# Optimization experiments

Hardware: AMD Instinct MI355X
Metric: run time of the kernel (lower is better)

## Reference

```python
import jax, jax.numpy as jnp
import numpy as np

EPS = 1e-5
TOPK_FRAC = 0.3
MIP = 16


def conv1x1(y, w, b):
    # y: (B, Cin, L, 1); w: (Cout, Cin); b: (Cout,)
    return jnp.einsum('oc,bclw->bolw', w, y) + b[None, :, None, None]


def mdca(x, conv1_w, conv1_b, bn_gamma, bn_beta, bn_mean, bn_var,
         convh_w, convh_b, convw_w, convw_b, convd1_w, convd1_b, convd2_w, convd2_b):
    B, C, H, W = x.shape
    x_h = jnp.mean(x, axis=3, keepdims=True)                       # (B,C,H,1)
    x_w = jnp.mean(x, axis=2, keepdims=True).transpose(0, 1, 3, 2)  # (B,C,W,1)
    x_d1 = jnp.rot90(x, k=-1, axes=(2, 3))                          # (B,C,W,H)
    x_d1 = jnp.mean(x_d1, axis=2, keepdims=True)                    # (B,C,1,H)
    x_d1 = jnp.rot90(x_d1, k=1, axes=(2, 3))                        # (B,C,H,1)
    x_d2 = jnp.rot90(x, k=1, axes=(2, 3))                           # (B,C,W,H)
    x_d2 = jnp.mean(x_d2, axis=2, keepdims=True)                    # (B,C,1,H)
    x_d2 = jnp.rot90(x_d2, k=-1, axes=(2, 3))                       # (B,C,H,1) -> size W along dim2 since H==W
    y = jnp.concatenate([x_h, x_w, x_d1, x_d2], axis=2)             # (B,C,H+W+H+W,1)
    y = conv1x1(y, conv1_w, conv1_b)                                # (B,mip,2H+2W,1)
    # BatchNorm (inference form with running stats)
    inv = jax.lax.rsqrt(bn_var + EPS)
    y = (y - bn_mean[None, :, None, None]) * (bn_gamma * inv)[None, :, None, None] + bn_beta[None, :, None, None]
    y = jax.nn.relu(y)
    xh, xw, xd1, xd2 = jnp.split(y, np.cumsum([H, W, H])[:3].tolist(), axis=2)
    xw = xw.transpose(0, 1, 3, 2)    # (B,mip,1,W)
    xd1 = xd1.transpose(0, 1, 3, 2)  # (B,mip,1,H)
    xd2 = xd2.transpose(0, 1, 3, 2)  # (B,mip,1,W)
    a_h = jax.nn.sigmoid(conv1x1(xh, convh_w, convh_b))    # (B,1,H,1)
    a_w = jax.nn.sigmoid(conv1x1(xw, convw_w, convw_b))    # (B,1,1,W)
    a_d1 = jax.nn.sigmoid(conv1x1(xd1, convd1_w, convd1_b))  # (B,1,1,H)
    a_d2 = jax.nn.sigmoid(conv1x1(xd2, convd2_w, convd2_b))  # (B,1,1,W)
    # broadcasting reproduces expand(-1,-1,H,-1); valid since H == W
    importance = a_w * a_h * a_d1 * a_d2                    # (B,1,H,W)
    return importance


def reference(x, conv1_w, conv1_b, bn_gamma, bn_beta, bn_mean, bn_var,
              convh_w, convh_b, convw_w, convw_b, convd1_w, convd1_b,
              convd2_w, convd2_b, sparsity_mask):
    B, C, H, W = x.shape
    imp = mdca(x, conv1_w, conv1_b, bn_gamma, bn_beta, bn_mean, bn_var,
               convh_w, convh_b, convw_w, convw_b, convd1_w, convd1_b, convd2_w, convd2_b)
    imp_flat = imp.reshape(B, -1)                               # (B,N)
    N = imp_flat.shape[1]
    scores = imp_flat[:, :, None] * imp_flat[:, None, :]        # (B,N,N) outer product
    scores = scores * jax.nn.sigmoid(sparsity_mask)
    k = max(1, int(N * TOPK_FRAC))
    vals, idx = jax.lax.top_k(scores, k)                        # (B,N,k)
    sparse = jnp.zeros_like(scores).at[
        jnp.arange(B)[:, None, None], jnp.arange(N)[None, :, None], idx
    ].set(vals)
    attn = jax.nn.softmax(sparse, axis=-1)                      # (B,N,N)
    x_seq = x.reshape(B, C, N).transpose(0, 2, 1)               # (B,N,C)
    out_seq = attn @ x_seq                                      # (B,N,C)
    return out_seq.transpose(0, 2, 1).reshape(B, C, H, W)


def setup_inputs():
    key = jax.random.key(0)
    ks = jax.random.split(key, 8)
    B, C, H, W = 2, 256, 64, 64
    s = 0.05
    return {
        'x': jax.random.normal(ks[0], (B, C, H, W), jnp.float32),
        'conv1_w': jax.random.normal(ks[1], (MIP, C), jnp.float32) * s,
        'conv1_b': jnp.zeros((MIP,), jnp.float32),
        'bn_gamma': jnp.ones((MIP,), jnp.float32),
        'bn_beta': jnp.zeros((MIP,), jnp.float32),
        'bn_mean': jnp.zeros((MIP,), jnp.float32),
        'bn_var': jnp.ones((MIP,), jnp.float32),
        'convh_w': jax.random.normal(ks[2], (1, MIP), jnp.float32) * s,
        'convh_b': jnp.zeros((1,), jnp.float32),
        'convw_w': jax.random.normal(ks[3], (1, MIP), jnp.float32) * s,
        'convw_b': jnp.zeros((1,), jnp.float32),
        'convd1_w': jax.random.normal(ks[4], (1, MIP), jnp.float32) * s,
        'convd1_b': jnp.zeros((1,), jnp.float32),
        'convd2_w': jax.random.normal(ks[5], (1, MIP), jnp.float32) * s,
        'convd2_b': jnp.zeros((1,), jnp.float32),
        'sparsity_mask': jnp.zeros((), jnp.float32),
    }
```

## Files before the change

### kernel.cpp

```cpp
#include <hip/hip_runtime.h>

#define B_ 2
#define C_ 256
#define HW_ 64
#define N_ 4096
#define K_SEL 1228
#define MIP_ 16

__device__ __forceinline__ float sigm(float z) { return 1.0f / (1.0f + expf(-z)); }

__global__ __launch_bounds__(256) void k_pre(const float* __restrict__ x,
                                             float* __restrict__ xhT) {
  __shared__ float rp[64][17];
  __shared__ float cp[16][65];
  int bc = blockIdx.x, t = threadIdx.x;
  int b = bc >> 8, c = bc & 255;
  const float* src = x + (size_t)bc * N_;
  int g = t >> 4, b16 = t & 15;
  float c0 = 0, c1 = 0, c2 = 0, c3 = 0;
  #pragma unroll
  for (int it = 0; it < 4; ++it) {
    int row = it * 16 + g;
    float4 v = *(const float4*)&src[row * 64 + b16 * 4];
    rp[row][b16] = v.x + v.y + v.z + v.w;
    c0 += v.x; c1 += v.y; c2 += v.z; c3 += v.w;
  }
  cp[g][b16 * 4 + 0] = c0;
  cp[g][b16 * 4 + 1] = c1;
  cp[g][b16 * 4 + 2] = c2;
  cp[g][b16 * 4 + 3] = c3;
  __syncthreads();
  if (t < 64) {
    float rs = 0;
    #pragma unroll
    for (int i = 0; i < 16; ++i) rs += rp[t][i];
    xhT[(((b * 2 + 0) * 64 + t) << 8) + c] = rs * (1.0f / 64.0f);
    float cs = 0;
    #pragma unroll
    for (int gg = 0; gg < 16; ++gg) cs += cp[gg][t];
    xhT[(((b * 2 + 1) * 64 + t) << 8) + c] = cs * (1.0f / 64.0f);
  }
}

__global__ __launch_bounds__(64) void k_conv(
    const float* __restrict__ xhT,
    const float* __restrict__ w1, const float* __restrict__ b1,
    const float* __restrict__ gam, const float* __restrict__ bet,
    const float* __restrict__ mea, const float* __restrict__ var,
    const float* __restrict__ wh, const float* __restrict__ bh,
    const float* __restrict__ ww, const float* __restrict__ bw,
    const float* __restrict__ wd1, const float* __restrict__ bd1,
    const float* __restrict__ wd2, const float* __restrict__ bd2,
    float* __restrict__ ahb, float* __restrict__ swb, float* __restrict__ sdb) {
  int blk = blockIdx.x;
  int l = threadIdx.x;
  const float* yrow = xhT + ((size_t)blk << 8);
  float4 v = *(const float4*)&yrow[l * 4];
  float r[MIP_];
  #pragma unroll
  for (int o = 0; o < MIP_; ++o) {
    float4 wv = *(const float4*)&w1[o * C_ + l * 4];
    float p = fmaf(v.x, wv.x, fmaf(v.y, wv.y, fmaf(v.z, wv.z, v.w * wv.w)));
    #pragma unroll
    for (int off = 32; off; off >>= 1) p += __shfl_xor(p, off, 64);
    r[o] = p;
  }
  float aH = bh[0], aW = bw[0], aD1 = bd1[0], aD2 = bd2[0];
  #pragma unroll
  for (int o = 0; o < MIP_; ++o) {
    float sc = gam[o] * rsqrtf(var[o] + 1e-5f);
    float y = r[o] + b1[o] - mea[o];
    float rr = fmaxf(fmaf(y, sc, bet[o]), 0.0f);
    aH = fmaf(wh[o], rr, aH);
    aW = fmaf(ww[o], rr, aW);
    aD1 = fmaf(wd1[o], rr, aD1);
    aD2 = fmaf(wd2[o], rr, aD2);
  }
  if (l == 0) {
    int seg = (blk >> 6) & 1, b = blk >> 7, pos = blk & 63;
    if (seg == 0) {
      ahb[b * HW_ + pos] = sigm(aH);
      sdb[b * HW_ + pos] = sigm(aD1) * sigm(aD2);
    } else {
      swb[b * HW_ + pos] = sigm(aW);
    }
  }
}

__global__ __launch_bounds__(256) void k_sel(
    const float* __restrict__ ahb, const float* __restrict__ swb,
    const float* __restrict__ sdb, const float* __restrict__ msk,
    float* __restrict__ fs, float2* __restrict__ ad) {
  __shared__ float ahs[HW_], sps[HW_];
  __shared__ int icomb[4];
  __shared__ float fmn[4], fmx[4];
  __shared__ float qpart[7][4];
  __shared__ float qsh[7];
  int b = blockIdx.x, t = threadIdx.x;
  if (t < HW_) {
    ahs[t] = ahb[b * HW_ + t];
    sps[t] = swb[b * HW_ + t] * sdb[b * HW_ + t];
  }
  __syncthreads();

  float v[16];
  #pragma unroll
  for (int k = 0; k < 16; ++k) {
    int j = k * 256 + t;
    v[k] = ahs[j >> 6] * sps[j & 63];
  }

  float mn = v[0], mx = v[0];
  #pragma unroll
  for (int k = 1; k < 16; ++k) { mn = fminf(mn, v[k]); mx = fmaxf(mx, v[k]); }
  #pragma unroll
  for (int o = 32; o; o >>= 1) {
    mn = fminf(mn, __shfl_xor(mn, o, 64));
    mx = fmaxf(mx, __shfl_xor(mx, o, 64));
  }
  if ((t & 63) == 0) { fmn[t >> 6] = mn; fmx[t >> 6] = mx; }
  __syncthreads();
  mn = fminf(fminf(fmn[0], fmn[1]), fminf(fmn[2], fmn[3]));
  mx = fmaxf(fmaxf(fmx[0], fmx[1]), fmaxf(fmx[2], fmx[3]));
  __syncthreads();

  unsigned lo = __float_as_uint(mn);
  unsigned hi = __float_as_uint(mx) + 1u;
  while (hi - lo > 8192u) {
    unsigned mid = lo + ((hi - lo) >> 1);
    float midf = __uint_as_float(mid);
    int cnt = 0;
    #pragma unroll
    for (int k = 0; k < 16; ++k) cnt += (v[k] >= midf) ? 1 : 0;
    #pragma unroll
    for (int o = 32; o; o >>= 1) cnt += __shfl_xor(cnt, o, 64);
    if ((t & 63) == 0) icomb[t >> 6] = cnt;
    __syncthreads();
    int total = icomb[0] + icomb[1] + icomb[2] + icomb[3];
    __syncthreads();
    if (total >= K_SEL) lo = mid; else hi = mid;
  }
  float thr = __uint_as_float(lo);
  float gm = sigm(msk[0]);

  float qm[7] = {0, 0, 0, 0, 0, 0, 0};
  float* fsb = fs + b * N_;
  #pragma unroll
  for (int k = 0; k < 16; ++k) {
    int j = k * 256 + t;
    float vv = v[k];
    bool sel = vv >= thr;
    fsb[j] = sel ? vv : 0.0f;
    if (sel) {
      float p = vv;
      qm[0] += p; p *= vv;
      qm[1] += p; p *= vv;
      qm[2] += p; p *= vv;
      qm[3] += p; p *= vv;
      qm[4] += p; p *= vv;
      qm[5] += p; p *= vv;
      qm[6] += p;
    }
  }
  #pragma unroll
  for (int m = 0; m < 7; ++m) {
    float s = qm[m];
    #pragma unroll
    for (int o = 32; o; o >>= 1) s += __shfl_xor(s, o, 64);
    if ((t & 63) == 0) qpart[m][t >> 6] = s;
  }
  __syncthreads();
  if (t < 7) {
    const float invf[7] = {1.0f, 0.5f, 1.0f / 6.0f, 1.0f / 24.0f,
                           1.0f / 120.0f, 1.0f / 720.0f, 1.0f / 5040.0f};
    qsh[t] = (qpart[t][0] + qpart[t][1] + qpart[t][2] + qpart[t][3]) * invf[t];
  }
  __syncthreads();

  float q1 = qsh[0], q2 = qsh[1], q3 = qsh[2], q4 = qsh[3];
  float q5 = qsh[4], q6 = qsh[5], q7 = qsh[6];
  float2* adb = ad + b * N_;
  #pragma unroll
  for (int k = 0; k < 16; ++k) {
    int j = k * 256 + t;
    float alpha = gm * v[k];
    float h = q7;
    h = fmaf(alpha, h, q6);
    h = fmaf(alpha, h, q5);
    h = fmaf(alpha, h, q4);
    h = fmaf(alpha, h, q3);
    h = fmaf(alpha, h, q2);
    h = fmaf(alpha, h, q1);
    float denom = fmaf(alpha, h, (float)N_);
    adb[j] = make_float2(alpha, 1.0f / denom);
  }
}

__global__ __launch_bounds__(256) void k_fin(const float* __restrict__ x,
                                             const float* __restrict__ fs,
                                             const float2* __restrict__ ad,
                                             float* __restrict__ out) {
  __shared__ float part[8][4];
  __shared__ float ps[8];
  int bc = blockIdx.x, b = bc >> 8, t = threadIdx.x;
  const float* xr = x + (size_t)bc * N_;
  const float* fr = fs + (size_t)b * N_;
  float pm[8] = {0, 0, 0, 0, 0, 0, 0, 0};
  #pragma unroll
  for (int it = 0; it < 4; ++it) {
    int j = it * 1024 + t * 4;
    float4 xv = *(const float4*)&xr[j];
    float4 fv = *(const float4*)&fr[j];
    const float xe[4] = {xv.x, xv.y, xv.z, xv.w};
    const float fe[4] = {fv.x, fv.y, fv.z, fv.w};
    #pragma unroll
    for (int e = 0; e < 4; ++e) {
      float xx = xe[e], vv = fe[e];
      pm[0] += xx;
      float p = vv;
      pm[1] = fmaf(p, xx, pm[1]); p *= vv;
      pm[2] = fmaf(p, xx, pm[2]); p *= vv;
      pm[3] = fmaf(p, xx, pm[3]); p *= vv;
      pm[4] = fmaf(p, xx, pm[4]); p *= vv;
      pm[5] = fmaf(p, xx, pm[5]); p *= vv;
      pm[6] = fmaf(p, xx, pm[6]); p *= vv;
      pm[7] = fmaf(p, xx, pm[7]);
    }
  }
  #pragma unroll
  for (int m = 0; m < 8; ++m) {
    float s = pm[m];
    #pragma unroll
    for (int o = 32; o; o >>= 1) s += __shfl_xor(s, o, 64);
    if ((t & 63) == 0) part[m][t >> 6] = s;
  }
  __syncthreads();
  if (t < 8) {
    const float invf[8] = {1.0f, 1.0f, 0.5f, 1.0f / 6.0f, 1.0f / 24.0f,
                           1.0f / 120.0f, 1.0f / 720.0f, 1.0f / 5040.0f};
    ps[t] = (part[t][0] + part[t][1] + part[t][2] + part[t][3]) * invf[t];
  }
  __syncthreads();
  float T = ps[0];
  float p1 = ps[1], p2 = ps[2], p3 = ps[3], p4 = ps[4];
  float p5 = ps[5], p6 = ps[6], p7 = ps[7];
  const float2* adb = ad + (size_t)b * N_;
  float* ob = out + (size_t)bc * N_;
  #pragma unroll 4
  for (int it = 0; it < 16; ++it) {
    int i = it * 256 + t;
    float2 a = adb[i];
    float h = p7;
    h = fmaf(a.x, h, p6);
    h = fmaf(a.x, h, p5);
    h = fmaf(a.x, h, p4);
    h = fmaf(a.x, h, p3);
    h = fmaf(a.x, h, p2);
    h = fmaf(a.x, h, p1);
    ob[i] = fmaf(a.x, h, T) * a.y;
  }
}

extern "C" void kernel_launch(void* const* d_in, const int* in_sizes, int n_in,
                              void* d_out, int out_size, void* d_ws, size_t ws_size,
                              hipStream_t stream) {
  (void)in_sizes; (void)n_in; (void)out_size; (void)ws_size;
  const float* x   = (const float*)d_in[0];
  const float* w1  = (const float*)d_in[1];
  const float* b1  = (const float*)d_in[2];
  const float* gam = (const float*)d_in[3];
  const float* bet = (const float*)d_in[4];
  const float* mea = (const float*)d_in[5];
  const float* var = (const float*)d_in[6];
  const float* wh  = (const float*)d_in[7];
  const float* bh  = (const float*)d_in[8];
  const float* ww  = (const float*)d_in[9];
  const float* bw  = (const float*)d_in[10];
  const float* wd1 = (const float*)d_in[11];
  const float* bd1 = (const float*)d_in[12];
  const float* wd2 = (const float*)d_in[13];
  const float* bd2 = (const float*)d_in[14];
  const float* msk = (const float*)d_in[15];
  float* out = (float*)d_out;

  float* ws  = (float*)d_ws;
  float* xhT = ws;
  float* ahb = ws + 65536;
  float* swb = ahb + 128;
  float* sdb = swb + 128;
  float* fs  = sdb + 128;
  float2* ad = (float2*)(fs + 8192);

  hipLaunchKernelGGL(k_pre, dim3(B_ * C_), dim3(256), 0, stream, x, xhT);
  hipLaunchKernelGGL(k_conv, dim3(B_ * 2 * HW_), dim3(64), 0, stream,
                     xhT, w1, b1, gam, bet, mea, var,
                     wh, bh, ww, bw, wd1, bd1, wd2, bd2, ahb, swb, sdb);
  hipLaunchKernelGGL(k_sel, dim3(B_), dim3(256), 0, stream,
                     ahb, swb, sdb, msk, fs, ad);
  hipLaunchKernelGGL(k_fin, dim3(B_ * C_), dim3(256), 0, stream,
                     x, fs, ad, out);
}
```

Before: 28.86 us.

## Fuse top-k selection kernel into final output kernel, recomputing threshold per block

Removes the separate two-block selection kernel and its fs/ad workspace round trips. Each of the 512 output blocks now rebuilds the 4096 importance values from the small per-row vectors, runs the binary-search threshold itself, and accumulates both the denominator and numerator moment sums in one pass over x. The output is written as float4 with a direct division. This trades one launch and a serial 2-block stage for redundant binary-search work and extra barriers in every block.

```diff
diff --git a/kernel.cpp b/kernel.cpp
--- a/kernel.cpp
+++ b/kernel.cpp
@@ -87,28 +87,41 @@
   }
 }
 
-__global__ __launch_bounds__(256) void k_sel(
+__global__ __launch_bounds__(256) void k_fin(
+    const float* __restrict__ x,
     const float* __restrict__ ahb, const float* __restrict__ swb,
     const float* __restrict__ sdb, const float* __restrict__ msk,
-    float* __restrict__ fs, float2* __restrict__ ad) {
+    float* __restrict__ out) {
   __shared__ float ahs[HW_], sps[HW_];
   __shared__ int icomb[4];
   __shared__ float fmn[4], fmx[4];
-  __shared__ float qpart[7][4];
-  __shared__ float qsh[7];
-  int b = blockIdx.x, t = threadIdx.x;
+  __shared__ float red[15][4];
+  __shared__ float ps[15];
+  int bc = blockIdx.x, b = bc >> 8, t = threadIdx.x;
+  const float* xr = x + (size_t)bc * N_;
+
+  float4 xv[4];
+  #pragma unroll
+  for (int it = 0; it < 4; ++it)
+    xv[it] = *(const float4*)&xr[it * 1024 + t * 4];
+
   if (t < HW_) {
     ahs[t] = ahb[b * HW_ + t];
     sps[t] = swb[b * HW_ + t] * sdb[b * HW_ + t];
   }
   __syncthreads();
 
+  float4 sp4 = *(const float4*)&sps[(t * 4) & 63];
+  const float spe[4] = {sp4.x, sp4.y, sp4.z, sp4.w};
+  float ahv[4];
+  #pragma unroll
+  for (int it = 0; it < 4; ++it) ahv[it] = ahs[it * 16 + (t >> 4)];
+
   float v[16];
   #pragma unroll
-  for (int k = 0; k < 16; ++k) {
-    int j = k * 256 + t;
-    v[k] = ahs[j >> 6] * sps[j & 63];
-  }
+  for (int it = 0; it < 4; ++it)
+    #pragma unroll
+    for (int e = 0; e < 4; ++e) v[it * 4 + e] = ahv[it] * spe[e];
 
   float mn = v[0], mx = v[0];
   #pragma unroll
@@ -122,7 +135,6 @@
   __syncthreads();
   mn = fminf(fminf(fmn[0], fmn[1]), fminf(fmn[2], fmn[3]));
   mx = fmaxf(fmaxf(fmx[0], fmx[1]), fmaxf(fmx[2], fmx[3]));
-  __syncthreads();
 
   unsigned lo = __float_as_uint(mn);
   unsigned hi = __float_as_uint(mx) + 1u;
@@ -143,121 +155,85 @@
   float thr = __uint_as_float(lo);
   float gm = sigm(msk[0]);
 
-  float qm[7] = {0, 0, 0, 0, 0, 0, 0};
-  float* fsb = fs + b * N_;
-  #pragma unroll
-  for (int k = 0; k < 16; ++k) {
-    int j = k * 256 + t;
-    float vv = v[k];
-    bool sel = vv >= thr;
-    fsb[j] = sel ? vv : 0.0f;
-    if (sel) {
-      float p = vv;
-      qm[0] += p; p *= vv;
-      qm[1] += p; p *= vv;
-      qm[2] += p; p *= vv;
-      qm[3] += p; p *= vv;
-      qm[4] += p; p *= vv;
-      qm[5] += p; p *= vv;
-      qm[6] += p;
+  float acc[15];
+  #pragma unroll
+  for (int m = 0; m < 15; ++m) acc[m] = 0.0f;
+  #pragma unroll
+  for (int it = 0; it < 4; ++it) {
+    const float xe[4] = {xv[it].x, xv[it].y, xv[it].z, xv[it].w};
+    #pragma unroll
+    for (int e = 0; e < 4; ++e) {
+      float vv = v[it * 4 + e];
+      float xx = xe[e];
+      acc[7] += xx;
+      if (vv >= thr) {
+        float p = vv;
+        acc[0] += p;
+        acc[8] = fmaf(p, xx, acc[8]); p *= vv;
+        acc[1] += p;
+        acc[9] = fmaf(p, xx, acc[9]); p *= vv;
+        acc[2] += p;
+        acc[10] = fmaf(p, xx, acc[10]); p *= vv;
+        acc[3] += p;
+        acc[11] = fmaf(p, xx, acc[11]); p *= vv;
+        acc[4] += p;
+        acc[12] = fmaf(p, xx, acc[12]); p *= vv;
+        acc[5] += p;
+        acc[13] = fmaf(p, xx, acc[13]); p *= vv;
+        acc[6] += p;
+        acc[14] = fmaf(p, xx, acc[14]);
+      }
     }
   }
   #pragma unroll
-  for (int m = 0; m < 7; ++m) {
-    float s = qm[m];
+  for (int m = 0; m < 15; ++m) {
+    float s = acc[m];
     #pragma unroll
     for (int o = 32; o; o >>= 1) s += __shfl_xor(s, o, 64);
-    if ((t & 63) == 0) qpart[m][t >> 6] = s;
-  }
-  __syncthreads();
-  if (t < 7) {
-    const float invf[7] = {1.0f, 0.5f, 1.0f / 6.0f, 1.0f / 24.0f,
-                           1.0f / 120.0f, 1.0f / 720.0f, 1.0f / 5040.0f};
-    qsh[t] = (qpart[t][0] + qpart[t][1] + qpart[t][2] + qpart[t][3]) * invf[t];
-  }
-  __syncthreads();
-
-  float q1 = qsh[0], q2 = qsh[1], q3 = qsh[2], q4 = qsh[3];
-  float q5 = qsh[4], q6 = qsh[5], q7 = qsh[6];
-  float2* adb = ad + b * N_;
-  #pragma unroll
-  for (int k = 0; k < 16; ++k) {
-    int j = k * 256 + t;
-    float alpha = gm * v[k];
-    float h = q7;
-    h = fmaf(alpha, h, q6);
-    h = fmaf(alpha, h, q5);
-    h = fmaf(alpha, h, q4);
-    h = fmaf(alpha, h, q3);
-    h = fmaf(alpha, h, q2);
-    h = fmaf(alpha, h, q1);
-    float denom = fmaf(alpha, h, (float)N_);
-    adb[j] = make_float2(alpha, 1.0f / denom);
-  }
-}
-
-__global__ __launch_bounds__(256) void k_fin(const float* __restrict__ x,
-                                             const float* __restrict__ fs,
-                                             const float2* __restrict__ ad,
-                                             float* __restrict__ out) {
-  __shared__ float part[8][4];
-  __shared__ float ps[8];
-  int bc = blockIdx.x, b = bc >> 8, t = threadIdx.x;
-  const float* xr = x + (size_t)bc * N_;
-  const float* fr = fs + (size_t)b * N_;
-  float pm[8] = {0, 0, 0, 0, 0, 0, 0, 0};
+    if ((t & 63) == 0) red[m][t >> 6] = s;
+  }
+  __syncthreads();
+  if (t < 15) {
+    const float invf[15] = {1.0f, 0.5f, 1.0f / 6.0f, 1.0f / 24.0f,
+                            1.0f / 120.0f, 1.0f / 720.0f, 1.0f / 5040.0f,
+                            1.0f,
+                            1.0f, 0.5f, 1.0f / 6.0f, 1.0f / 24.0f,
+                            1.0f / 120.0f, 1.0f / 720.0f, 1.0f / 5040.0f};
+    ps[t] = (red[t][0] + red[t][1] + red[t][2] + red[t][3]) * invf[t];
+  }
+  __syncthreads();
+  float q1 = ps[0], q2 = ps[1], q3 = ps[2], q4 = ps[3];
+  float q5 = ps[4], q6 = ps[5], q7 = ps[6];
+  float T = ps[7];
+  float p1 = ps[8], p2 = ps[9], p3 = ps[10], p4 = ps[11];
+  float p5 = ps[12], p6 = ps[13], p7 = ps[14];
+
+  float* ob = out + (size_t)bc * N_;
   #pragma unroll
   for (int it = 0; it < 4; ++it) {
-    int j = it * 1024 + t * 4;
-    float4 xv = *(const float4*)&xr[j];
-    float4 fv = *(const float4*)&fr[j];
-    const float xe[4] = {xv.x, xv.y, xv.z, xv.w};
-    const float fe[4] = {fv.x, fv.y, fv.z, fv.w};
+    float o4[4];
     #pragma unroll
     for (int e = 0; e < 4; ++e) {
-      float xx = xe[e], vv = fe[e];
-      pm[0] += xx;
-      float p = vv;
-      pm[1] = fmaf(p, xx, pm[1]); p *= vv;
-      pm[2] = fmaf(p, xx, pm[2]); p *= vv;
-      pm[3] = fmaf(p, xx, pm[3]); p *= vv;
-      pm[4] = fmaf(p, xx, pm[4]); p *= vv;
-      pm[5] = fmaf(p, xx, pm[5]); p *= vv;
-      pm[6] = fmaf(p, xx, pm[6]); p *= vv;
-      pm[7] = fmaf(p, xx, pm[7]);
+      float alpha = gm * v[it * 4 + e];
+      float hn = p7;
+      hn = fmaf(alpha, hn, p6);
+      hn = fmaf(alpha, hn, p5);
+      hn = fmaf(alpha, hn, p4);
+      hn = fmaf(alpha, hn, p3);
+      hn = fmaf(alpha, hn, p2);
+      hn = fmaf(alpha, hn, p1);
+      float numer = fmaf(alpha, hn, T);
+      float hd = q7;
+      hd = fmaf(alpha, hd, q6);
+      hd = fmaf(alpha, hd, q5);
+      hd = fmaf(alpha, hd, q4);
+      hd = fmaf(alpha, hd, q3);
+      hd = fmaf(alpha, hd, q2);
+      hd = fmaf(alpha, hd, q1);
+      float denom = fmaf(alpha, hd, (float)N_);
+      o4[e] = numer / denom;
     }
-  }
-  #pragma unroll
-  for (int m = 0; m < 8; ++m) {
-    float s = pm[m];
-    #pragma unroll
-    for (int o = 32; o; o >>= 1) s += __shfl_xor(s, o, 64);
-    if ((t & 63) == 0) part[m][t >> 6] = s;
-  }
-  __syncthreads();
-  if (t < 8) {
-    const float invf[8] = {1.0f, 1.0f, 0.5f, 1.0f / 6.0f, 1.0f / 24.0f,
-                           1.0f / 120.0f, 1.0f / 720.0f, 1.0f / 5040.0f};
-    ps[t] = (part[t][0] + part[t][1] + part[t][2] + part[t][3]) * invf[t];
-  }
-  __syncthreads();
-  float T = ps[0];
-  float p1 = ps[1], p2 = ps[2], p3 = ps[3], p4 = ps[4];
-  float p5 = ps[5], p6 = ps[6], p7 = ps[7];
-  const float2* adb = ad + (size_t)b * N_;
-  float* ob = out + (size_t)bc * N_;
-  #pragma unroll 4
-  for (int it = 0; it < 16; ++it) {
-    int i = it * 256 + t;
-    float2 a = adb[i];
-    float h = p7;
-    h = fmaf(a.x, h, p6);
-    h = fmaf(a.x, h, p5);
-    h = fmaf(a.x, h, p4);
-    h = fmaf(a.x, h, p3);
-    h = fmaf(a.x, h, p2);
-    h = fmaf(a.x, h, p1);
-    ob[i] = fmaf(a.x, h, T) * a.y;
+    *(float4*)&ob[it * 1024 + t * 4] = make_float4(o4[0], o4[1], o4[2], o4[3]);
   }
 }
 
@@ -288,15 +264,11 @@
   float* ahb = ws + 65536;
   float* swb = ahb + 128;
   float* sdb = swb + 128;
-  float* fs  = sdb + 128;
-  float2* ad = (float2*)(fs + 8192);
 
   hipLaunchKernelGGL(k_pre, dim3(B_ * C_), dim3(256), 0, stream, x, xhT);
   hipLaunchKernelGGL(k_conv, dim3(B_ * 2 * HW_), dim3(64), 0, stream,
                      xhT, w1, b1, gam, bet, mea, var,
                      wh, bh, ww, bw, wd1, bd1, wd2, bd2, ahb, swb, sdb);
-  hipLaunchKernelGGL(k_sel, dim3(B_), dim3(256), 0, stream,
-                     ahb, swb, sdb, msk, fs, ad);
   hipLaunchKernelGGL(k_fin, dim3(B_ * C_), dim3(256), 0, stream,
-                     x, fs, ad, out);
-}
+                     x, ahb, swb, sdb, msk, out);
+}
```

After: 25.63 us. -11.2%, faster.
